# Kernel tuning notes

Hardware: AMD Instinct MI355X
Metric: run time of the kernel (lower is better)

## Reference

```python
import jax, jax.numpy as jnp
import numpy as np

B, T, D, E = 8, 2048, 256, 4
D_E = D // E


def setup_inputs() -> dict:
    key = jax.random.key(0)
    ks = jax.random.split(key, 12)
    s = 1.0 / np.sqrt(D)
    x = jax.random.normal(ks[0], (B, T, D), dtype=jnp.float32)
    # ensure max(seq_len) == T so the padded input matches this_batch_padlen
    seq_len = jnp.concatenate([
        jax.random.randint(ks[1], (B - 1,), T // 2, T),
        jnp.array([T]),
    ]).astype(jnp.int32)
    return {
        "x": x,
        "seq_len": seq_len,
        "wq": jax.random.uniform(ks[2], (D, D), jnp.float32, -s, s),
        "bq": jax.random.uniform(ks[3], (D,), jnp.float32, -s, s),
        "wk": jax.random.uniform(ks[4], (D, D), jnp.float32, -s, s),
        "bk": jax.random.uniform(ks[5], (D,), jnp.float32, -s, s),
        "wv": jax.random.uniform(ks[6], (D, D), jnp.float32, -s, s),
        "bv": jax.random.uniform(ks[7], (D,), jnp.float32, -s, s),
        "wo": jax.random.uniform(ks[8], (D, D), jnp.float32, -s, s),
        "bo": jax.random.uniform(ks[9], (D,), jnp.float32, -s, s),
        "theta": jnp.array([50.0], dtype=jnp.float32),
    }


def _split_heads(y):
    # faithful to torch: [B,T,D] -> permute(0,2,1) -> [B,D,T] -> reshape(B*E, T, D_E)
    return jnp.transpose(y, (0, 2, 1)).reshape(B * E, T, D_E)


def reference(x, seq_len, wq, bq, wk, bk, wv, bv, wo, bo, theta):
    Q = _split_heads(x @ wq.T + bq)          # [B*E, T, D_E]
    K = _split_heads(x @ wk.T + bk)          # [B*E, T, D_E]
    V = _split_heads(x @ wv.T + bv)          # [B*E, T, D_E]

    # padding mask: zero out query rows (and key cols) past seq_len[i]
    pos = jnp.arange(T)
    valid = (pos[None, :] < seq_len[:, None])                 # [B, T]
    mask_q = jnp.repeat(valid, E, axis=0).astype(Q.dtype)     # [B*E, T]
    Q = Q * mask_q[:, :, None]
    K = K * mask_q[:, :, None]

    scale = jnp.sqrt(jnp.float32(T))
    att = jnp.einsum('bqd,bkd->bqk', Q, K) / scale            # [B*E, T, T]

    # Gaussian positional penalty (is_punish=True)
    tpos = jnp.arange(T, dtype=jnp.float32)
    diff = tpos[None, :] - tpos[:, None]                      # j - i
    punish = jnp.exp(-(diff ** 2) / (theta[0] ** 2))          # [T, T]
    att = att * punish[None, :, :]

    att = jnp.where(att == 0.0, jnp.float32(-2e20), att)
    att = jax.nn.softmax(att, axis=2)

    ctx = jnp.einsum('bqk,bkd->bqd', att, V)                  # [B*E, T, D_E]
    # faithful inverse of _split_heads: permute(0,2,1)->reshape(B,D,T)->permute
    ctx = jnp.transpose(jnp.transpose(ctx, (0, 2, 1)).reshape(B, D, T), (0, 2, 1))
    A = ctx @ wo.T + bo
    return A + x
```

## Files before the change

### kernel.cpp

```cpp
#include <hip/hip_runtime.h>
#include <math.h>
#include <stdint.h>

#define B_SZ   8
#define T_SEQ  2048
#define DIM    256
#define NH     32
#define DE     64
#define BAND   509
#define M_ROWS (B_SZ * T_SEQ)

typedef __attribute__((ext_vector_type(8))) short short8;
typedef __attribute__((ext_vector_type(4))) float floatx4;
typedef unsigned short ushort_t;

__device__ __forceinline__ ushort_t f2bf(float x) {
    unsigned u = __float_as_uint(x);
    u += 0x7fffu + ((u >> 16) & 1u);
    return (ushort_t)(u >> 16);
}
__device__ __forceinline__ float bf2f(ushort_t b) {
    return __uint_as_float(((unsigned)b) << 16);
}
__device__ __forceinline__ unsigned pack2(float a, float b) {
    return (unsigned)f2bf(a) | ((unsigned)f2bf(b) << 16);
}

__device__ __forceinline__ double pd_exact(int d, float th) {
    float df  = (float)d;
    float arg = (-(df * df)) / (th * th);
    double pdd = exp((double)arg);
    if (pdd < 1.17549435082228751e-38)
        return rint(pdd * 0x1p149) * 0x1p-149;
    return (double)(float)pdd;
}

__global__ __launch_bounds__(256) void prep_kernel(
    const float* __restrict__ x,
    const float* __restrict__ wq, const float* __restrict__ wk,
    const float* __restrict__ wv, const float* __restrict__ wo,
    const float* __restrict__ theta,
    ushort_t* __restrict__ xb, ushort_t* __restrict__ wb,
    float* __restrict__ thr_g, float* __restrict__ pdf_g)
{
    const int bid = blockIdx.x, tid = threadIdx.x;
    if (bid < 2048) {
        size_t i8 = ((size_t)bid * 256 + tid) * 8;
        float4 a = *(const float4*)(x + i8);
        float4 b = *(const float4*)(x + i8 + 4);
        uint4 o;
        o.x = pack2(a.x, a.y); o.y = pack2(a.z, a.w);
        o.z = pack2(b.x, b.y); o.w = pack2(b.z, b.w);
        *(uint4*)(xb + i8) = o;
    } else if (bid < 2176) {
        size_t w8 = ((size_t)(bid - 2048) * 256 + tid) * 8;
        int which = (int)(w8 >> 16);
        const float* src = (which == 0) ? wq : (which == 1) ? wk : (which == 2) ? wv : wo;
        size_t off = w8 & 65535;
        float4 a = *(const float4*)(src + off);
        float4 b = *(const float4*)(src + off + 4);
        uint4 o;
        o.x = pack2(a.x, a.y); o.y = pack2(a.z, a.w);
        o.z = pack2(b.x, b.y); o.w = pack2(b.z, b.w);
        *(uint4*)(wb + w8) = o;
    } else {
        int i = (bid - 2176) * 256 + tid;
        float th = theta[0];
        if (i < 384) pdf_g[i] = (float)pd_exact(i, th);
        if (i < 288) {
            double pdv = pd_exact(321 + i, th);
            thr_g[i] = (pdv == 0.0) ? __builtin_inff() : (float)(0x1p-150 / pdv);
        }
    }
}

__global__ __launch_bounds__(256, 2) void proj_qkv_mfma(
    const ushort_t* __restrict__ xb, const ushort_t* __restrict__ wb,
    const float* __restrict__ bq, const float* __restrict__ bk,
    const float* __restrict__ bv, const int* __restrict__ seq_len,
    ushort_t* __restrict__ Qh, ushort_t* __restrict__ Kh, ushort_t* __restrict__ Vh)
{
    __shared__ __align__(16) ushort_t Ls[4][64][68];
    const int wave = threadIdx.x >> 6, lane = threadIdx.x & 63;
    const int quad = lane >> 4, l15 = lane & 15;
    const int task = blockIdx.x * 4 + wave;
    const int nt64 = task % 12;
    const int mstrip = task / 12;
    const int mode = nt64 >> 2;
    const int nloc_base = (nt64 & 3) * 64;
    const ushort_t* Wp = wb + (size_t)mode * 65536;
    const int m0 = mstrip * 64;
    const int bb = m0 >> 11;
    const int th0 = (m0 >> 6) & 31;
    const int sl = seq_len[bb];
    ushort_t* outp = (mode == 0) ? Qh : (mode == 1) ? Kh : Vh;
    const float* bias = (mode == 0) ? bq : (mode == 1) ? bk : bv;
    const int hh = bb * 4 + (nloc_base >> 6);
    const float oscale = (mode == 0) ? 0.022097086912079612f : 1.0f;

    short8 Bf[4][8];
    #pragma unroll
    for (int nt = 0; nt < 4; ++nt) {
        int nrow = nloc_base + nt * 16 + l15;
        #pragma unroll
        for (int ks = 0; ks < 8; ++ks)
            Bf[nt][ks] = *(const short8*)(Wp + (size_t)nrow * 256 + ks * 32 + quad * 8);
    }
    float bias4[4];
    #pragma unroll
    for (int nt = 0; nt < 4; ++nt) bias4[nt] = bias[nloc_base + nt * 16 + l15];

    short8 Acur[8];
    #pragma unroll
    for (int ks = 0; ks < 8; ++ks)
        Acur[ks] = *(const short8*)(xb + (size_t)(m0 + l15) * 256 + ks * 32 + quad * 8);

    #pragma unroll
    for (int mb = 0; mb < 4; ++mb) {
        const int mb0 = m0 + mb * 16;
        short8 Anext[8];
        if (mb < 3) {
            #pragma unroll
            for (int ks = 0; ks < 8; ++ks)
                Anext[ks] = *(const short8*)(xb + (size_t)(mb0 + 16 + l15) * 256 + ks * 32 + quad * 8);
        }
        floatx4 acc[4];
        #pragma unroll
        for (int nt = 0; nt < 4; ++nt) acc[nt] = (floatx4){0.f, 0.f, 0.f, 0.f};
        #pragma unroll
        for (int ks = 0; ks < 8; ++ks)
            #pragma unroll
            for (int nt = 0; nt < 4; ++nt)
                acc[nt] = __builtin_amdgcn_mfma_f32_16x16x32_bf16(Acur[ks], Bf[nt][ks], acc[nt], 0, 0, 0);
        #pragma unroll
        for (int nt = 0; nt < 4; ++nt) {
            float v0 = (acc[nt][0] + bias4[nt]) * oscale;
            float v1 = (acc[nt][1] + bias4[nt]) * oscale;
            float v2 = (acc[nt][2] + bias4[nt]) * oscale;
            float v3 = (acc[nt][3] + bias4[nt]) * oscale;
            uint2 pk; pk.x = pack2(v0, v1); pk.y = pack2(v2, v3);
            *(uint2*)&Ls[wave][nt * 16 + l15][mb * 16 + quad * 4] = pk;
        }
        #pragma unroll
        for (int ks = 0; ks < 8; ++ks) Acur[ks] = Anext[ks];
    }

    #pragma unroll
    for (int s = 0; s < 16; ++s) {
        int dl = s * 4 + quad;
        int e0 = l15 * 4;
        uint2 pk = *(const uint2*)&Ls[wave][dl][e0];
        int q = dl * 32 + th0;
        if (mode <= 1 && q >= sl) { pk.x = 0u; pk.y = 0u; }
        *(uint2*)(outp + (((size_t)hh * T_SEQ + q) << 6) + e0) = pk;
    }
}

__global__ __launch_bounds__(256) void vtrans_kernel(const ushort_t* __restrict__ Vh,
                                                     ushort_t* __restrict__ VTp)
{
    __shared__ ushort_t Vs[256][66];
    const int tid = threadIdx.x;
    const int h = blockIdx.x >> 3, chunk = blockIdx.x & 7;
    const ushort_t* src = Vh + ((size_t)(h * T_SEQ + chunk * 256)) * DE;
    #pragma unroll
    for (int rep = 0; rep < 8; ++rep) {
        int f = rep * 256 + tid;
        int row = f >> 3, c8 = (f & 7) * 8;
        *(uint4*)&Vs[row][c8] = *(const uint4*)(src + (size_t)row * DE + c8);
    }
    __syncthreads();
    const int w = tid >> 6, lane = tid & 63;
    const int half = lane >> 5;
    const int c32 = lane & 31;
    const int cbase = c32 * 8;
    const int blk = cbase >> 6;
    const int cin = cbase & 63;
    #pragma unroll
    for (int rr = 0; rr < 8; ++rr) {
        int e = w * 16 + rr * 2 + half;
        ushort_t tmp[8];
        #pragma unroll
        for (int t = 0; t < 8; ++t) {
            int ci = cin + t;
            int j = blk * 64 + (ci >> 2) + 16 * (ci & 3);
            tmp[t] = Vs[j][e];
        }
        *(uint4*)(VTp + ((size_t)(h * DE + e)) * T_SEQ + chunk * 256 + cbase) = *(uint4*)tmp;
    }
}

__global__ __launch_bounds__(256) void meanv_partial(const ushort_t* __restrict__ Vh,
                                                     float* __restrict__ mv) {
    __shared__ float red[32][72];
    const int blk = blockIdx.x;
    const int h = blk >> 3, chunk = blk & 7;
    const int tid = threadIdx.x;
    const int r0 = tid >> 3;
    const int es = (tid & 7) * 8;
    const ushort_t* p = Vh + ((size_t)h * T_SEQ + chunk * 256 + r0) * DE + es;
    float s[8] = {};
    #pragma unroll
    for (int k = 0; k < 8; ++k) {
        uint4 u = *(const uint4*)(p + (size_t)k * 32 * DE);
        const ushort_t* w = (const ushort_t*)&u;
        #pragma unroll
        for (int i = 0; i < 8; ++i) s[i] += bf2f(w[i]);
    }
    #pragma unroll
    for (int i = 0; i < 8; ++i) red[r0][es + i] = s[i];
    __syncthreads();
    if (tid < 64) {
        float t = 0.f;
        #pragma unroll
        for (int g = 0; g < 32; ++g) t += red[g][tid];
        atomicAdd(&mv[h * DE + tid], t);
    }
}

__global__ __launch_bounds__(256) void attn_mfma_kernel(
    const ushort_t* __restrict__ Qh, const ushort_t* __restrict__ Kh,
    const ushort_t* __restrict__ VTp, const float* __restrict__ thr_g,
    const float* __restrict__ pdf_g, const float* __restrict__ mvs,
    const int* __restrict__ seq_len, ushort_t* __restrict__ ctxb)
{
    __shared__ ushort_t Ks [64][72];
    __shared__ ushort_t VTs[64][72];
    __shared__ ushort_t Ps [4][16][72];
    __shared__ float pdfs[384];
    __shared__ float thrs[288];

    const int tid  = threadIdx.x;
    const int wave = tid >> 6;
    const int lane = tid & 63;
    const int quad = lane >> 4;
    const int l15  = lane & 15;
    const int bid   = blockIdx.x;
    const int inner = bid >> 3;
    const int h  = ((inner >> 5) << 3) | (bid & 7);
    const int q0 = (inner & 31) * 64;
    const int b  = h >> 2;
    const int sl = seq_len[b];
    const float invT = 1.0f / (float)T_SEQ;
    ushort_t* outbase = ctxb + ((size_t)b * T_SEQ + q0) * DIM + (size_t)(h & 3) * 64;

    if (q0 >= sl) {
        #pragma unroll
        for (int nt = 0; nt < 4; ++nt) {
            ushort_t mval = f2bf(mvs[h * DE + l15 + 16 * nt] * invT);
            #pragma unroll
            for (int r = 0; r < 4; ++r)
                outbase[(size_t)(wave * 16 + quad * 4 + r) * DIM + l15 + 16 * nt] = mval;
        }
        return;
    }

    for (int i = tid; i < 384; i += 256) pdfs[i] = pdf_g[i];
    for (int i = tid; i < 288; i += 256) thrs[i] = thr_g[i];

    short8 qa0, qa1;
    {
        const ushort_t* qp = Qh + ((size_t)h * T_SEQ + q0 + wave * 16 + l15) * DE + quad * 8;
        qa0 = *(const short8*)(qp);
        qa1 = *(const short8*)(qp + 32);
    }

    float l_acc[4] = {0.f, 0.f, 0.f, 0.f};
    floatx4 cacc[4];
    #pragma unroll
    for (int nt = 0; nt < 4; ++nt) cacc[nt] = (floatx4){0.f, 0.f, 0.f, 0.f};

    int jlo = q0 - BAND;      if (jlo < 0) jlo = 0;
    int jhi = q0 + 63 + BAND; if (jhi > sl - 1) jhi = sl - 1;
    const int jt0 = jlo >> 6, jt1 = jhi >> 6;

    const int krow = tid >> 3;
    const int kc8  = (tid & 7) * 8;
    const ushort_t* Kbp = Kh + (size_t)h * T_SEQ * DE;
    const ushort_t* Vbp = VTp + (size_t)h * DE * T_SEQ;
    uint4 kpre0, kpre1, vpre0, vpre1;
    {
        const int j0 = jt0 << 6;
        kpre0 = *(const uint4*)(Kbp + (size_t)(j0 + krow) * DE + kc8);
        kpre1 = *(const uint4*)(Kbp + (size_t)(j0 + krow + 32) * DE + kc8);
        vpre0 = *(const uint4*)(Vbp + (size_t)krow * T_SEQ + j0 + kc8);
        vpre1 = *(const uint4*)(Vbp + (size_t)(krow + 32) * T_SEQ + j0 + kc8);
    }

    for (int jt = jt0; jt <= jt1; ++jt) {
        const int j0 = jt << 6;
        __syncthreads();
        *(uint4*)&Ks[krow][kc8]       = kpre0;
        *(uint4*)&Ks[krow + 32][kc8]  = kpre1;
        *(uint4*)&VTs[krow][kc8]      = vpre0;
        *(uint4*)&VTs[krow + 32][kc8] = vpre1;
        __syncthreads();
        if (jt < jt1) {
            const int jn = j0 + 64;
            kpre0 = *(const uint4*)(Kbp + (size_t)(jn + krow) * DE + kc8);
            kpre1 = *(const uint4*)(Kbp + (size_t)(jn + krow + 32) * DE + kc8);
            vpre0 = *(const uint4*)(Vbp + (size_t)krow * T_SEQ + jn + kc8);
            vpre1 = *(const uint4*)(Vbp + (size_t)(krow + 32) * T_SEQ + jn + kc8);
        }

        floatx4 S[4];
        #pragma unroll
        for (int nt = 0; nt < 4; ++nt) {
            short8 kb0 = *(const short8*)&Ks[l15 + 16 * nt][quad * 8];
            short8 kb1 = *(const short8*)&Ks[l15 + 16 * nt][32 + quad * 8];
            floatx4 z = {0.f, 0.f, 0.f, 0.f};
            z = __builtin_amdgcn_mfma_f32_16x16x32_bf16(qa0, kb0, z, 0, 0, 0);
            z = __builtin_amdgcn_mfma_f32_16x16x32_bf16(qa1, kb1, z, 0, 0, 0);
            S[nt] = z;
        }

        const int off = j0 - q0;
        float p[4][4];
        if (off >= -320 && off <= 320) {
            #pragma unroll
            for (int nt = 0; nt < 4; ++nt) {
                int jg = j0 + l15 + 16 * nt;
                bool jv = (jg < sl);
                #pragma unroll
                for (int r = 0; r < 4; ++r) {
                    int dd = jg - (q0 + wave * 16 + quad * 4 + r);
                    dd = dd < 0 ? -dd : dd;
                    float av = S[nt][r] * pdfs[dd];
                    av = jv ? av : -1e30f;
                    p[nt][r] = __expf(av);
                }
            }
        } else {
            #pragma unroll
            for (int nt = 0; nt < 4; ++nt) {
                int jg = j0 + l15 + 16 * nt;
                #pragma unroll
                for (int r = 0; r < 4; ++r) {
                    int dd = jg - (q0 + wave * 16 + quad * 4 + r);
                    dd = dd < 0 ? -dd : dd;
                    p[nt][r] = (fabsf(S[nt][r]) > thrs[dd - 321]) ? 1.0f : 0.0f;
                }
            }
        }

        #pragma unroll
        for (int r = 0; r < 4; ++r) {
            l_acc[r] += (p[0][r] + p[1][r]) + (p[2][r] + p[3][r]);
            uint2 pk;
            pk.x = pack2(p[0][r], p[1][r]);
            pk.y = pack2(p[2][r], p[3][r]);
            *(uint2*)&Ps[wave][quad * 4 + r][l15 * 4] = pk;
        }
        short8 pa0 = *(const short8*)&Ps[wave][l15][quad * 8];
        short8 pa1 = *(const short8*)&Ps[wave][l15][32 + quad * 8];
        #pragma unroll
        for (int nt = 0; nt < 4; ++nt) {
            short8 vb0 = *(const short8*)&VTs[l15 + 16 * nt][quad * 8];
            short8 vb1 = *(const short8*)&VTs[l15 + 16 * nt][32 + quad * 8];
            floatx4 c = cacc[nt];
            c = __builtin_amdgcn_mfma_f32_16x16x32_bf16(pa0, vb0, c, 0, 0, 0);
            c = __builtin_amdgcn_mfma_f32_16x16x32_bf16(pa1, vb1, c, 0, 0, 0);
            cacc[nt] = c;
        }
    }

    #pragma unroll
    for (int r = 0; r < 4; ++r) {
        float lv = l_acc[r];
        #pragma unroll
        for (int o = 1; o <= 8; o <<= 1) lv += __shfl_xor(lv, o);
        l_acc[r] = 1.0f / lv;
    }
    #pragma unroll
    for (int nt = 0; nt < 4; ++nt) {
        #pragma unroll
        for (int r = 0; r < 4; ++r) {
            int row = wave * 16 + quad * 4 + r;
            int qg = q0 + row;
            float o = cacc[nt][r] * l_acc[r];
            if (qg >= sl) o = mvs[h * DE + l15 + 16 * nt] * invT;
            outbase[(size_t)row * DIM + l15 + 16 * nt] = f2bf(o);
        }
    }
}

__global__ __launch_bounds__(256, 2) void proj_o_mfma(
    const ushort_t* __restrict__ ctx, const ushort_t* __restrict__ wb,
    const float* __restrict__ bo, const float* __restrict__ x,
    float* __restrict__ out)
{
    const int wave = threadIdx.x >> 6, lane = threadIdx.x & 63;
    const int quad = lane >> 4, l15 = lane & 15;
    const int task = blockIdx.x * 4 + wave;
    const int nt64 = task & 3;
    const int mstrip = task >> 2;
    const int n0 = nt64 * 64;
    const ushort_t* Wp = wb + (size_t)3 * 65536;
    const int m0 = mstrip * 64;

    short8 Bf[4][8];
    #pragma unroll
    for (int nt = 0; nt < 4; ++nt) {
        int nrow = n0 + nt * 16 + l15;
        #pragma unroll
        for (int ks = 0; ks < 8; ++ks)
            Bf[nt][ks] = *(const short8*)(Wp + (size_t)nrow * 256 + ks * 32 + quad * 8);
    }
    float bias4[4];
    #pragma unroll
    for (int nt = 0; nt < 4; ++nt) bias4[nt] = bo[n0 + nt * 16 + l15];

    short8 Acur[8];
    #pragma unroll
    for (int ks = 0; ks < 8; ++ks)
        Acur[ks] = *(const short8*)(ctx + (size_t)(m0 + l15) * 256 + ks * 32 + quad * 8);

    #pragma unroll
    for (int mb = 0; mb < 4; ++mb) {
        const int mb0 = m0 + mb * 16;
        short8 Anext[8];
        if (mb < 3) {
            #pragma unroll
            for (int ks = 0; ks < 8; ++ks)
                Anext[ks] = *(const short8*)(ctx + (size_t)(mb0 + 16 + l15) * 256 + ks * 32 + quad * 8);
        }
        floatx4 acc[4];
        #pragma unroll
        for (int nt = 0; nt < 4; ++nt) acc[nt] = (floatx4){0.f, 0.f, 0.f, 0.f};
        #pragma unroll
        for (int ks = 0; ks < 8; ++ks)
            #pragma unroll
            for (int nt = 0; nt < 4; ++nt)
                acc[nt] = __builtin_amdgcn_mfma_f32_16x16x32_bf16(Acur[ks], Bf[nt][ks], acc[nt], 0, 0, 0);
        #pragma unroll
        for (int nt = 0; nt < 4; ++nt) {
            int d = n0 + nt * 16 + l15;
            #pragma unroll
            for (int r = 0; r < 4; ++r) {
                size_t mi = (size_t)(mb0 + quad * 4 + r) * 256 + d;
                out[mi] = acc[nt][r] + bias4[nt] + x[mi];
            }
        }
        #pragma unroll
        for (int ks = 0; ks < 8; ++ks) Acur[ks] = Anext[ks];
    }
}

extern "C" void kernel_launch(void* const* d_in, const int* in_sizes, int n_in,
                              void* d_out, int out_size, void* d_ws, size_t ws_size,
                              hipStream_t stream)
{
    (void)in_sizes; (void)n_in; (void)out_size; (void)ws_size;
    const float* x  = (const float*)d_in[0];
    const int*   sl = (const int*)d_in[1];
    const float* wq = (const float*)d_in[2];
    const float* bq = (const float*)d_in[3];
    const float* wk = (const float*)d_in[4];
    const float* bk = (const float*)d_in[5];
    const float* wv = (const float*)d_in[6];
    const float* bv = (const float*)d_in[7];
    const float* wo = (const float*)d_in[8];
    const float* bo = (const float*)d_in[9];
    const float* th = (const float*)d_in[10];
    float* out = (float*)d_out;

    char* ws = (char*)d_ws;
    const size_t SZH = (size_t)M_ROWS * DIM * sizeof(ushort_t);
    ushort_t* xb  = (ushort_t*)(ws);
    ushort_t* wb  = (ushort_t*)(ws + SZH);
    ushort_t* Qh  = (ushort_t*)(ws + SZH + 524288);
    ushort_t* Kh  = (ushort_t*)(ws + 2*SZH + 524288);
    ushort_t* Vh  = (ushort_t*)(ws + 3*SZH + 524288);
    ushort_t* VTp = (ushort_t*)(ws + 4*SZH + 524288);
    ushort_t* Cb  = (ushort_t*)(ws + 5*SZH + 524288);
    float*    Mv  = (float*)   (ws + 6*SZH + 524288);
    float*    Thr = (float*)   (ws + 6*SZH + 524288 + 8192);
    float*    Pdf = (float*)   (ws + 6*SZH + 524288 + 12288);

    hipMemsetAsync(Mv, 0, NH * DE * sizeof(float), stream);
    prep_kernel<<<dim3(2178), dim3(256), 0, stream>>>(x, wq, wk, wv, wo, th, xb, wb, Thr, Pdf);
    proj_qkv_mfma<<<dim3(768), dim3(256), 0, stream>>>(xb, wb, bq, bk, bv, sl, Qh, Kh, Vh);
    vtrans_kernel<<<dim3(NH * 8), dim3(256), 0, stream>>>(Vh, VTp);
    meanv_partial<<<dim3(256), dim3(256), 0, stream>>>(Vh, Mv);
    attn_mfma_kernel<<<dim3(1024), dim3(256), 0, stream>>>(Qh, Kh, VTp, Thr, Pdf, Mv, sl, Cb);
    proj_o_mfma<<<dim3(256), dim3(256), 0, stream>>>(Cb, wb, bo, x, out);
}
```

Before: 185.4 us.

## Share ctx tile via LDS across waves in output projection, double block count

The output projection now stages a 32-row ctx tile in shared memory, which all four waves reuse, each covering a different 64-column slice of the output. Before, every wave loaded its own 64-row strip from global memory. The grid doubles to 512 blocks, each handling 32 rows. This cuts redundant global reads of ctx and gives more parallelism, at the cost of a barrier, the LDS traffic and losing the register prefetch pipelining.

```diff
diff --git a/kernel.cpp b/kernel.cpp
--- a/kernel.cpp
+++ b/kernel.cpp
@@ -389,14 +389,20 @@
     const float* __restrict__ bo, const float* __restrict__ x,
     float* __restrict__ out)
 {
-    const int wave = threadIdx.x >> 6, lane = threadIdx.x & 63;
+    __shared__ __align__(16) ushort_t As[32][264];
+    const int tid = threadIdx.x;
+    const int wave = tid >> 6, lane = tid & 63;
     const int quad = lane >> 4, l15 = lane & 15;
-    const int task = blockIdx.x * 4 + wave;
-    const int nt64 = task & 3;
-    const int mstrip = task >> 2;
-    const int n0 = nt64 * 64;
+    const int m0 = blockIdx.x * 32;
+    const int n0 = wave * 64;
     const ushort_t* Wp = wb + (size_t)3 * 65536;
-    const int m0 = mstrip * 64;
+
+    #pragma unroll
+    for (int rep = 0; rep < 4; ++rep) {
+        int f = rep * 256 + tid;
+        int row = f >> 5, c8 = (f & 31) * 8;
+        *(uint4*)&As[row][c8] = *(const uint4*)(ctx + (size_t)(m0 + row) * 256 + c8);
+    }
 
     short8 Bf[4][8];
     #pragma unroll
@@ -410,20 +416,14 @@
     #pragma unroll
     for (int nt = 0; nt < 4; ++nt) bias4[nt] = bo[n0 + nt * 16 + l15];
 
-    short8 Acur[8];
-    #pragma unroll
-    for (int ks = 0; ks < 8; ++ks)
-        Acur[ks] = *(const short8*)(ctx + (size_t)(m0 + l15) * 256 + ks * 32 + quad * 8);
-
-    #pragma unroll
-    for (int mb = 0; mb < 4; ++mb) {
-        const int mb0 = m0 + mb * 16;
-        short8 Anext[8];
-        if (mb < 3) {
-            #pragma unroll
-            for (int ks = 0; ks < 8; ++ks)
-                Anext[ks] = *(const short8*)(ctx + (size_t)(mb0 + 16 + l15) * 256 + ks * 32 + quad * 8);
-        }
+    __syncthreads();
+
+    #pragma unroll
+    for (int mb = 0; mb < 2; ++mb) {
+        short8 Af[8];
+        #pragma unroll
+        for (int ks = 0; ks < 8; ++ks)
+            Af[ks] = *(const short8*)&As[mb * 16 + l15][ks * 32 + quad * 8];
         floatx4 acc[4];
         #pragma unroll
         for (int nt = 0; nt < 4; ++nt) acc[nt] = (floatx4){0.f, 0.f, 0.f, 0.f};
@@ -431,18 +431,16 @@
         for (int ks = 0; ks < 8; ++ks)
             #pragma unroll
             for (int nt = 0; nt < 4; ++nt)
-                acc[nt] = __builtin_amdgcn_mfma_f32_16x16x32_bf16(Acur[ks], Bf[nt][ks], acc[nt], 0, 0, 0);
+                acc[nt] = __builtin_amdgcn_mfma_f32_16x16x32_bf16(Af[ks], Bf[nt][ks], acc[nt], 0, 0, 0);
         #pragma unroll
         for (int nt = 0; nt < 4; ++nt) {
             int d = n0 + nt * 16 + l15;
             #pragma unroll
             for (int r = 0; r < 4; ++r) {
-                size_t mi = (size_t)(mb0 + quad * 4 + r) * 256 + d;
+                size_t mi = (size_t)(m0 + mb * 16 + quad * 4 + r) * 256 + d;
                 out[mi] = acc[nt][r] + bias4[nt] + x[mi];
             }
         }
-        #pragma unroll
-        for (int ks = 0; ks < 8; ++ks) Acur[ks] = Anext[ks];
     }
 }
 
@@ -483,5 +481,5 @@
     vtrans_kernel<<<dim3(NH * 8), dim3(256), 0, stream>>>(Vh, VTp);
     meanv_partial<<<dim3(256), dim3(256), 0, stream>>>(Vh, Mv);
     attn_mfma_kernel<<<dim3(1024), dim3(256), 0, stream>>>(Qh, Kh, VTp, Thr, Pdf, Mv, sl, Cb);
-    proj_o_mfma<<<dim3(256), dim3(256), 0, stream>>>(Cb, wb, bo, x, out);
-}
+    proj_o_mfma<<<dim3(512), dim3(256), 0, stream>>>(Cb, wb, bo, x, out);
+}
```

Result: faster. 179.3 us (-3.3%).
